# Kernel optimization log

Measured on AMD Instinct MI355X. Metric: run time of the kernel, lower is better.

Reference implementation:

```python
import jax, jax.numpy as jnp
import numpy as np

N = 50000          # nodes
E = 1_600_000      # directed edges (avg degree 32)
C_IN = 512
C_OUT = 64
H1, F1 = 8, 8      # conv1: heads=8, out per head=8
H2 = 1             # conv2: heads_2=1, concat=False
NEG_SLOPE = 0.2    # GATConv default leaky_relu slope
ELU_ALPHA = 0.2    # F.elu(..., alpha=0.2) in forward


def _glorot(key, shape):
    fan_in, fan_out = shape[0], shape[-1]
    lim = jnp.sqrt(6.0 / (fan_in + fan_out))
    return jax.random.uniform(key, shape, jnp.float32, -lim, lim)


def setup_inputs() -> dict:
    key = jax.random.key(0)
    ks = jax.random.split(key, 12)
    x = jax.random.normal(ks[0], (N, C_IN), jnp.float32)
    edge_index = jax.random.randint(ks[1], (2, E), 0, N, jnp.int32)
    # conv1 params
    W1 = _glorot(ks[2], (C_IN, H1 * F1))
    att_src1 = _glorot(ks[3], (H1, F1))
    att_dst1 = _glorot(ks[4], (H1, F1))
    b1 = jnp.zeros((H1 * F1,), jnp.float32)
    # conv2 params (concat=False, heads=1)
    W2 = _glorot(ks[5], (H1 * F1, H2 * C_OUT))
    att_src2 = _glorot(ks[6], (H2, C_OUT))
    att_dst2 = _glorot(ks[7], (H2, C_OUT))
    b2 = jnp.zeros((C_OUT,), jnp.float32)
    return dict(x=x, edge_index=edge_index, W1=W1, att_src1=att_src1,
                att_dst1=att_dst1, b1=b1, W2=W2, att_src2=att_src2,
                att_dst2=att_dst2, b2=b2)


def gat_conv(x, src, dst, W, att_src, att_dst, bias, concat):
    """PyG GATConv (self-loops already appended to src/dst). Eval mode (no dropout)."""
    n = x.shape[0]
    H, F = att_src.shape
    h = (x @ W).reshape(n, H, F)                       # [N,H,F]
    a_src = jnp.sum(h * att_src, axis=-1)              # [N,H]
    a_dst = jnp.sum(h * att_dst, axis=-1)              # [N,H]
    e = jax.nn.leaky_relu(a_src[src] + a_dst[dst], NEG_SLOPE)  # [E',H]
    # segment softmax over incoming edges of each destination node
    m = jax.ops.segment_max(e, dst, num_segments=n)    # [N,H]
    m = jnp.where(jnp.isfinite(m), m, 0.0)
    ex = jnp.exp(e - m[dst])
    denom = jax.ops.segment_sum(ex, dst, num_segments=n)
    alpha = ex / (denom[dst] + 1e-16)                  # [E',H]
    msg = h[src] * alpha[:, :, None]                   # [E',H,F]
    out = jax.ops.segment_sum(msg, dst, num_segments=n)  # [N,H,F]
    out = out.reshape(n, H * F) if concat else out.mean(axis=1)
    return out + bias


def reference(x, edge_index, W1, att_src1, att_dst1, b1,
              W2, att_src2, att_dst2, b2):
    # add self loops once (GATConv default add_self_loops=True)
    loop = jnp.arange(N, dtype=edge_index.dtype)
    src = jnp.concatenate([edge_index[0], loop])
    dst = jnp.concatenate([edge_index[1], loop])
    # dropout layers are identity in eval mode
    h = gat_conv(x, src, dst, W1, att_src1, att_dst1, b1, concat=True)
    h = jax.nn.elu(h, alpha=ELU_ALPHA)
    out = gat_conv(h, src, dst, W2, att_src2, att_dst2, b2, concat=False)
    return out
```

## Files before the change

### kernel.cpp

```cpp
#include <hip/hip_runtime.h>
#include <hip/hip_bf16.h>
#include <hip/hip_fp16.h>

constexpr int NN   = 50000;
constexpr int NE   = 1600000;
constexpr int CIN  = 512;
constexpr int DH   = 64;
constexpr int H1N  = 8;

constexpr int NB     = 98;
constexpr int TILE   = 8192;
constexpr int NTILES = (NE + TILE - 1) / TILE;
constexpr int BCAP   = 20480;

typedef __attribute__((ext_vector_type(8))) short bf16x8v;
typedef __attribute__((ext_vector_type(4))) float f32x4v;

__device__ __forceinline__ float bf(unsigned short u) {
    union { unsigned int i; float f; } v; v.i = ((unsigned int)u) << 16; return v.f;
}
__device__ __forceinline__ float lrelu(float x) { return fmaxf(x, 0.2f * x); }
__device__ __forceinline__ float ldf(const unsigned short* p, size_t i, bool f32) {
    return f32 ? ((const float*)p)[i] : bf(p[i]);
}
__device__ __forceinline__ unsigned short f2bf(float f) {
    union { float f; unsigned int u; } v; v.f = f;
    unsigned int r = (v.u + 0x7fff + ((v.u >> 16) & 1)) >> 16;
    return (unsigned short)r;
}

__global__ __launch_bounds__(256) void gat_detect(const unsigned short* __restrict__ W1,
                                                  int* __restrict__ flag) {
    __shared__ int cnt;
    if (threadIdx.x == 0) cnt = 0;
    __syncthreads();
    int local = 0;
    for (int i = threadIdx.x; i < 4096; i += 256) {
        unsigned short u = W1[i];
        int e = (u >> 7) & 0xFF;
        if (e >= 140) local++;
    }
    atomicAdd(&cnt, local);
    __syncthreads();
    if (threadIdx.x == 0) flag[0] = (cnt > 100) ? 1 : 0;
}


__global__ __launch_bounds__(256) void gat_bucketA(const int* __restrict__ src,
                                                   const int* __restrict__ dst,
                                                   int* __restrict__ gcnt,
                                                   unsigned int* __restrict__ bucketed) {
    __shared__ int hist[NB];
    __shared__ int cur[NB];
    int t = threadIdx.x;
    if (t < NB) hist[t] = 0;
    __syncthreads();
    int base = blockIdx.x * TILE;
    for (int i = t; i < TILE; i += 256) {
        int e = base + i;
        if (e < NE) atomicAdd(&hist[dst[e] >> 9], 1);
    }
    __syncthreads();
    if (t < NB) cur[t] = hist[t] ? atomicAdd(&gcnt[t], hist[t]) : 0;
    __syncthreads();
    for (int i = t; i < TILE; i += 256) {
        int e = base + i;
        if (e < NE) {
            int d = dst[e];
            int b = d >> 9;
            int p = atomicAdd(&cur[b], 1);
            if (p < BCAP)
                bucketed[(size_t)b * BCAP + p] =
                    ((unsigned int)(d & 511) << 16) | (unsigned int)src[e];
        }
    }
}

__global__ __launch_bounds__(128) void gat_bucketscan(const int* __restrict__ gcnt,
                                                      int* __restrict__ boff,
                                                      int* __restrict__ row_ptr) {
    __shared__ int s[128];
    int t = threadIdx.x;
    s[t] = (t < NB) ? gcnt[t] : 0;
    __syncthreads();
    for (int off = 1; off < 128; off <<= 1) {
        int x = s[t];
        int add = (t >= off) ? s[t - off] : 0;
        __syncthreads();
        s[t] = x + add;
        __syncthreads();
    }
    if (t <= NB) boff[t] = (t == 0) ? 0 : s[t - 1];
    if (t == 0) row_ptr[NN] = NE;
}

__global__ __launch_bounds__(256) void gat_bucketB(const unsigned int* __restrict__ bucketed,
                                                   const int* __restrict__ gcnt,
                                                   const int* __restrict__ boff,
                                                   int* __restrict__ row_ptr,
                                                   int* __restrict__ col_idx) {
    __shared__ int hist[512];
    __shared__ int sums[256];
    int t = threadIdx.x;
    int b = blockIdx.x;
    int e0 = boff[b];
    int cnt = gcnt[b]; if (cnt > BCAP) cnt = BCAP;
    const unsigned int* bb = bucketed + (size_t)b * BCAP;
    hist[t] = 0; hist[t + 256] = 0;
    __syncthreads();
    for (int i = t; i < cnt; i += 256)
        atomicAdd(&hist[bb[i] >> 16], 1);
    __syncthreads();
    int a0 = hist[2 * t], a1 = hist[2 * t + 1];
    sums[t] = a0 + a1;
    __syncthreads();
    for (int off = 1; off < 256; off <<= 1) {
        int x = sums[t];
        int add = (t >= off) ? sums[t - off] : 0;
        __syncthreads();
        sums[t] = x + add;
        __syncthreads();
    }
    int excl = (t == 0) ? 0 : sums[t - 1];
    hist[2 * t]     = excl;
    hist[2 * t + 1] = excl + a0;
    int node0 = b << 9;
    if (node0 + 2 * t     < NN) row_ptr[node0 + 2 * t]     = e0 + excl;
    if (node0 + 2 * t + 1 < NN) row_ptr[node0 + 2 * t + 1] = e0 + excl + a0;
    __syncthreads();
    for (int i = t; i < cnt; i += 256) {
        unsigned int pk = bb[i];
        int p = atomicAdd(&hist[pk >> 16], 1);
        col_idx[e0 + p] = (int)(pk & 0xFFFFu);
    }
}


__global__ __launch_bounds__(256) void gat_maxcol(const float* __restrict__ v, int n, int H,
                                                  unsigned int* __restrict__ out) {
    __shared__ float red[256];
    int t = threadIdx.x;
    float mx = -3.4e38f;
    for (int idx = blockIdx.x * 256 + t; idx < n; idx += gridDim.x * 256)
        mx = fmaxf(mx, v[idx]);
    red[t] = mx;
    __syncthreads();
    for (int off = 128; off >= H; off >>= 1) {
        if (t < off) red[t] = fmaxf(red[t], red[t + off]);
        __syncthreads();
    }
    if (t < H) {
        union { float f; unsigned int u; } b; b.f = red[t];
        unsigned int enc = (b.u & 0x80000000u) ? ~b.u : (b.u | 0x80000000u);
        atomicMax(&out[t], enc);
    }
}

__device__ __forceinline__ float gdecode(unsigned int u) {
    union { unsigned int u; float f; } d;
    d.u = (u & 0x80000000u) ? (u ^ 0x80000000u) : ~u;
    return d.f;
}


__global__ __launch_bounds__(256) void gat_transW(const unsigned short* __restrict__ W1,
                                                  const int* __restrict__ flag,
                                                  unsigned short* __restrict__ wts) {
    int idx = blockIdx.x * 256 + threadIdx.x;
    int n = idx >> 9, k = idx & 511;
    if (flag[0] == 0) {
        int o  = n * 1024 + k * 2;
        int os = o ^ ((n & 7) << 4);
        wts[os >> 1] = W1[(size_t)k * DH + n];
    } else {
        float v = ((const float*)W1)[(size_t)k * DH + n];
        unsigned short hi = f2bf(v);
        union { unsigned int u; float f; } hf; hf.u = ((unsigned int)hi) << 16;
        unsigned short lo = f2bf(v - hf.f);
        int q = k >> 7, kk = k & 127;
        int o = q * 32768 + n * 256 + ((kk * 2) ^ ((n & 7) << 4));
        wts[o >> 1]             = hi;
        wts[(o + 16384) >> 1]   = lo;
    }
}


__global__ __launch_bounds__(256) void gat_transW2(const unsigned short* __restrict__ W2,
                                                   const int* __restrict__ flag,
                                                   unsigned short* __restrict__ wts2) {
    int idx = blockIdx.x * 256 + threadIdx.x;
    if (idx >= 4096) return;
    int n = idx & 63, k = idx >> 6;
    unsigned short hi, lo;
    if (flag[0] == 0) {
        hi = W2[(size_t)k * DH + n];
        lo = 0;
    } else {
        float v = ((const float*)W2)[(size_t)k * DH + n];
        hi = f2bf(v);
        union { unsigned int u; float f; } hf; hf.u = ((unsigned int)hi) << 16;
        lo = f2bf(v - hf.f);
    }
    int o = n * 128 + ((k * 2) ^ ((n & 7) << 4));
    wts2[o >> 1]            = hi;
    wts2[(o + 8192) >> 1]   = lo;
}


__global__ __launch_bounds__(256) void gat_gemm1_mfma(const unsigned short* __restrict__ x,
                                                      const unsigned short* __restrict__ wts,
                                                      const unsigned short* __restrict__ as1,
                                                      const unsigned short* __restrict__ ad1,
                                                      const int* __restrict__ flag,
                                                      __half* __restrict__ h1h,
                                                      float* __restrict__ a_s1,
                                                      float* __restrict__ a_d1) {
    if (flag[0] != 0) return;
    __shared__ __align__(16) unsigned short wl[32768];
    int t = threadIdx.x;
#pragma unroll
    for (int it = 0; it < 16; ++it) {
        int c = it * 256 + t;
        *(uint4*)((char*)wl + c * 16) = *(const uint4*)((const char*)wts + c * 16);
    }
    __syncthreads();

    int lane = t & 63, wv = t >> 6;
    int g = lane >> 4;
    int r = lane & 15;
    int chunk = blockIdx.x * 4 + wv;
    if (chunk * 16 >= NN) return;
    int rowbase = chunk * 16;

    int vbase = r * 1024;
    int gx = g * 16;
    int xr = (r & 7) << 4;

    const char* xrow = (const char*)x + ((size_t)(rowbase + r) * CIN + g * 8) * 2;

    f32x4v acc[4];
#pragma unroll
    for (int nt = 0; nt < 4; ++nt) acc[nt] = (f32x4v){0.f, 0.f, 0.f, 0.f};

#pragma unroll 4
    for (int s = 0; s < 16; ++s) {
        union { uint4 u; bf16x8v v; } a;
        a.u = *(const uint4*)(xrow + s * 64);
        int o = vbase + ((s * 64 + gx) ^ xr);
        const char* bp = (const char*)wl + o;
#pragma unroll
        for (int nt = 0; nt < 4; ++nt) {
            union { uint4 u; bf16x8v v; } bv;
            bv.u = *(const uint4*)(bp + nt * 16384);
            acc[nt] = __builtin_amdgcn_mfma_f32_16x16x32_bf16(a.v, bv.v, acc[nt], 0, 0, 0);
        }
    }

    float avs[4], avd[4];
#pragma unroll
    for (int nt = 0; nt < 4; ++nt) {
        avs[nt] = bf(as1[nt * 16 + r]);
        avd[nt] = bf(ad1[nt * 16 + r]);
    }

#pragma unroll
    for (int nt = 0; nt < 4; ++nt) {
#pragma unroll
        for (int i = 0; i < 4; ++i) {
            int row = rowbase + g * 4 + i;
            float v = acc[nt][i];
            h1h[(size_t)row * DH + nt * 16 + r] = __float2half(v);
            float ps = v * avs[nt];
            float pd = v * avd[nt];
            ps += __shfl_xor(ps, 1, 64); ps += __shfl_xor(ps, 2, 64); ps += __shfl_xor(ps, 4, 64);
            pd += __shfl_xor(pd, 1, 64); pd += __shfl_xor(pd, 2, 64); pd += __shfl_xor(pd, 4, 64);
            if ((r & 7) == 0) {
                int head = nt * 2 + (r >> 3);
                a_s1[row * H1N + head] = ps;
                a_d1[row * H1N + head] = pd;
            }
        }
    }
}


__global__ __launch_bounds__(256) void gat_gemm1_mfma_f32(const float* __restrict__ x,
                                                          const unsigned short* __restrict__ wts,
                                                          const float* __restrict__ as1,
                                                          const float* __restrict__ ad1,
                                                          const int* __restrict__ flag,
                                                          __half* __restrict__ h1h,
                                                          float* __restrict__ a_s1,
                                                          float* __restrict__ a_d1) {
    if (flag[0] == 0) return;
    __shared__ __align__(16) unsigned short wl[16384];
    int t = threadIdx.x;
    int lane = t & 63, wv = t >> 6;
    int g = lane >> 4;
    int r = lane & 15;
    int chunk = blockIdx.x * 4 + wv;
    bool active = (chunk * 16 < NN);
    int rowbase = (active ? chunk : 0) * 16;

    int vbase = r * 256;
    int xr = (r & 7) << 4;

    const float* xrow = x + (size_t)(rowbase + r) * CIN + g * 8;

    f32x4v acc[4];
#pragma unroll
    for (int nt = 0; nt < 4; ++nt) acc[nt] = (f32x4v){0.f, 0.f, 0.f, 0.f};

    for (int q = 0; q < 4; ++q) {
        if (q) __syncthreads();
        const uint4* gsrc = (const uint4*)((const char*)wts + q * 32768);
#pragma unroll
        for (int it = 0; it < 8; ++it)
            ((uint4*)wl)[it * 256 + t] = gsrc[it * 256 + t];
        __syncthreads();

#pragma unroll
        for (int s = 0; s < 4; ++s) {
            const float4* xp = (const float4*)(xrow + q * 128 + s * 32);
            float4 v0 = xp[0], v1 = xp[1];
            float xv[8] = {v0.x, v0.y, v0.z, v0.w, v1.x, v1.y, v1.z, v1.w};
            union { unsigned short u[8]; bf16x8v v; } ahi, alo;
#pragma unroll
            for (int i2 = 0; i2 < 8; ++i2) {
                union { float f; unsigned int u; } xb; xb.f = xv[i2];
                unsigned int hb = xb.u & 0xffff0000u;
                union { unsigned int u; float f; } hf; hf.u = hb;
                ahi.u[i2] = (unsigned short)(xb.u >> 16);
                alo.u[i2] = f2bf(xv[i2] - hf.f);
            }
            int o = vbase + ((s * 64 + g * 16) ^ xr);
#pragma unroll
            for (int nt = 0; nt < 4; ++nt) {
                union { uint4 u; bf16x8v v; } bhi, blo;
                bhi.u = *(const uint4*)((const char*)wl + nt * 4096 + o);
                blo.u = *(const uint4*)((const char*)wl + 16384 + nt * 4096 + o);
                acc[nt] = __builtin_amdgcn_mfma_f32_16x16x32_bf16(ahi.v, bhi.v, acc[nt], 0, 0, 0);
                acc[nt] = __builtin_amdgcn_mfma_f32_16x16x32_bf16(ahi.v, blo.v, acc[nt], 0, 0, 0);
                acc[nt] = __builtin_amdgcn_mfma_f32_16x16x32_bf16(alo.v, bhi.v, acc[nt], 0, 0, 0);
            }
        }
    }

    if (!active) return;

    float avs[4], avd[4];
#pragma unroll
    for (int nt = 0; nt < 4; ++nt) {
        avs[nt] = as1[nt * 16 + r];
        avd[nt] = ad1[nt * 16 + r];
    }

#pragma unroll
    for (int nt = 0; nt < 4; ++nt) {
#pragma unroll
        for (int i = 0; i < 4; ++i) {
            int row = rowbase + g * 4 + i;
            float v = acc[nt][i];
            h1h[(size_t)row * DH + nt * 16 + r] = __float2half(v);
            float ps = v * avs[nt];
            float pd = v * avd[nt];
            ps += __shfl_xor(ps, 1, 64); ps += __shfl_xor(ps, 2, 64); ps += __shfl_xor(ps, 4, 64);
            pd += __shfl_xor(pd, 1, 64); pd += __shfl_xor(pd, 2, 64); pd += __shfl_xor(pd, 4, 64);
            if ((r & 7) == 0) {
                int head = nt * 2 + (r >> 3);
                a_s1[row * H1N + head] = ps;
                a_d1[row * H1N + head] = pd;
            }
        }
    }
}


__global__ __launch_bounds__(256) void gat_agg1(const int* __restrict__ row_ptr,
                                                const int* __restrict__ col_idx,
                                                const float* __restrict__ a_s1,
                                                const float* __restrict__ a_d1,
                                                const unsigned int* __restrict__ Gsu,
                                                const __half* __restrict__ h1h,
                                                const unsigned short* __restrict__ b1,
                                                const int* __restrict__ flag,
                                                float* __restrict__ hout) {
    const bool f32 = (flag[0] != 0);
    int i = (blockIdx.x * 256 + threadIdx.x) >> 6;
    int lane = threadIdx.x & 63;
    if (i >= NN) return;
    int ek = lane & 3;
    int eh = (lane >> 2) & 7;
    int wbase = (lane >> 3) << 2;

    float adst = a_d1[i * H1N + eh];
    float m = lrelu(gdecode(Gsu[eh]) + adst);

    int jb = row_ptr[i], je = row_ptr[i + 1];
    int deg = je - jb;
    int myidx = (lane < deg) ? col_idx[jb + lane] : 0;

    float wself = __expf(lrelu(a_s1[i * H1N + eh] + adst) - m);
    float denp = (ek == 0) ? wself : 0.f;
    float wsb = __shfl(wself, wbase, 64);
    float acc = wsb * __half2float(h1h[(size_t)i * DH + lane]);

    for (int j0 = 0; j0 < deg; j0 += 4) {
        int s0, s1, s2, s3, se;
        bool vE = (j0 + ek) < deg;
        if (j0 < 64) {
            s0 = __shfl(myidx, j0,     64);
            s1 = __shfl(myidx, j0 + 1, 64);
            s2 = __shfl(myidx, j0 + 2, 64);
            s3 = __shfl(myidx, j0 + 3, 64);
            se = __shfl(myidx, j0 + ek, 64);
        } else {
            int j1 = j0 + 1 < deg ? j0 + 1 : j0;
            int j2 = j0 + 2 < deg ? j0 + 2 : j0;
            int j3 = j0 + 3 < deg ? j0 + 3 : j0;
            int jve = vE ? (j0 + ek) : j0;
            s0 = col_idx[jb + j0];
            s1 = col_idx[jb + j1];
            s2 = col_idx[jb + j2];
            s3 = col_idx[jb + j3];
            se = col_idx[jb + jve];
        }
        float w = __expf(lrelu(a_s1[se * H1N + eh] + adst) - m);
        w = vE ? w : 0.f;
        denp += w;
        float w0 = __shfl(w, wbase + 0, 64);
        float w1 = __shfl(w, wbase + 1, 64);
        float w2 = __shfl(w, wbase + 2, 64);
        float w3 = __shfl(w, wbase + 3, 64);
        float r0 = __half2float(h1h[(size_t)s0 * DH + lane]);
        float r1 = __half2float(h1h[(size_t)s1 * DH + lane]);
        float r2 = __half2float(h1h[(size_t)s2 * DH + lane]);
        float r3 = __half2float(h1h[(size_t)s3 * DH + lane]);
        acc += (w0 * r0 + w1 * r1) + (w2 * r2 + w3 * r3);
    }
    denp += __shfl_xor(denp, 1, 64);
    denp += __shfl_xor(denp, 2, 64);
    float denom = __shfl(denp, wbase, 64);

    float val = acc / denom + ldf(b1, lane, f32);
    val = val > 0.f ? val : 0.2f * (__expf(val) - 1.f);
    hout[(size_t)i * DH + lane] = val;
}


__global__ __launch_bounds__(256) void gat_gemm2_mfma(const float* __restrict__ hin,
                                                      const unsigned short* __restrict__ wts2,
                                                      const unsigned short* __restrict__ as2,
                                                      const unsigned short* __restrict__ ad2,
                                                      const int* __restrict__ flag,
                                                      __half* __restrict__ h2h,
                                                      float* __restrict__ a_s2,
                                                      float* __restrict__ a_d2) {
    __shared__ __align__(16) unsigned short wl[8192];
    const bool f32 = (flag[0] != 0);
    int t = threadIdx.x;
#pragma unroll
    for (int it = 0; it < 4; ++it)
        ((uint4*)wl)[it * 256 + t] = ((const uint4*)wts2)[it * 256 + t];
    __syncthreads();

    int lane = t & 63, wv = t >> 6;
    int g = lane >> 4;
    int r = lane & 15;
    int chunk = blockIdx.x * 4 + wv;
    if (chunk * 16 >= NN) return;
    int rowbase = chunk * 16;

    int vbase = r * 128;
    int xr = (r & 7) << 4;

    const float* xrow = hin + (size_t)(rowbase + r) * DH + g * 8;

    f32x4v acc[4];
#pragma unroll
    for (int nt = 0; nt < 4; ++nt) acc[nt] = (f32x4v){0.f, 0.f, 0.f, 0.f};

#pragma unroll
    for (int s = 0; s < 2; ++s) {
        const float4* xp = (const float4*)(xrow + s * 32);
        float4 v0 = xp[0], v1 = xp[1];
        float xv[8] = {v0.x, v0.y, v0.z, v0.w, v1.x, v1.y, v1.z, v1.w};
        union { unsigned short u[8]; bf16x8v v; } ahi, alo;
#pragma unroll
        for (int i2 = 0; i2 < 8; ++i2) {
            union { float f; unsigned int u; } xb; xb.f = xv[i2];
            unsigned int hb = xb.u & 0xffff0000u;
            union { unsigned int u; float f; } hf; hf.u = hb;
            ahi.u[i2] = (unsigned short)(xb.u >> 16);
            alo.u[i2] = f2bf(xv[i2] - hf.f);
        }
        int o = vbase + ((s * 64 + g * 16) ^ xr);
#pragma unroll
        for (int nt = 0; nt < 4; ++nt) {
            union { uint4 u; bf16x8v v; } bhi, blo;
            bhi.u = *(const uint4*)((const char*)wl + nt * 2048 + o);
            blo.u = *(const uint4*)((const char*)wl + 8192 + nt * 2048 + o);
            acc[nt] = __builtin_amdgcn_mfma_f32_16x16x32_bf16(ahi.v, bhi.v, acc[nt], 0, 0, 0);
            acc[nt] = __builtin_amdgcn_mfma_f32_16x16x32_bf16(ahi.v, blo.v, acc[nt], 0, 0, 0);
            acc[nt] = __builtin_amdgcn_mfma_f32_16x16x32_bf16(alo.v, bhi.v, acc[nt], 0, 0, 0);
        }
    }

    float avs[4], avd[4];
#pragma unroll
    for (int nt = 0; nt < 4; ++nt) {
        avs[nt] = ldf(as2, nt * 16 + r, f32);
        avd[nt] = ldf(ad2, nt * 16 + r, f32);
    }

#pragma unroll
    for (int i = 0; i < 4; ++i) {
        int row = rowbase + g * 4 + i;
        float ps = 0.f, pd = 0.f;
#pragma unroll
        for (int nt = 0; nt < 4; ++nt) {
            float v = acc[nt][i];
            h2h[(size_t)row * DH + nt * 16 + r] = __float2half(v);
            ps += v * avs[nt];
            pd += v * avd[nt];
        }
        ps += __shfl_xor(ps, 1, 64); ps += __shfl_xor(ps, 2, 64);
        ps += __shfl_xor(ps, 4, 64); ps += __shfl_xor(ps, 8, 64);
        pd += __shfl_xor(pd, 1, 64); pd += __shfl_xor(pd, 2, 64);
        pd += __shfl_xor(pd, 4, 64); pd += __shfl_xor(pd, 8, 64);
        if (r == 0) { a_s2[row] = ps; a_d2[row] = pd; }
    }
}


__global__ __launch_bounds__(256) void gat_agg2(const int* __restrict__ row_ptr,
                                                const int* __restrict__ col_idx,
                                                const float* __restrict__ a_s2,
                                                const float* __restrict__ a_d2,
                                                const unsigned int* __restrict__ Gsu2,
                                                const __half* __restrict__ h2h,
                                                const unsigned short* __restrict__ b2,
                                                const int* __restrict__ flag,
                                                void* __restrict__ out) {
    const bool f32 = (flag[0] != 0);
    int i = (blockIdx.x * 256 + threadIdx.x) >> 6;
    int lane = threadIdx.x & 63;
    if (i >= NN) return;
    int ek = lane & 3;

    float adst = a_d2[i];
    float m = lrelu(gdecode(Gsu2[0]) + adst);

    int jb = row_ptr[i], je = row_ptr[i + 1];
    int deg = je - jb;
    int myidx = (lane < deg) ? col_idx[jb + lane] : 0;

    float wself = __expf(lrelu(a_s2[i] + adst) - m);
    float denp = (ek == 0) ? wself : 0.f;
    float acc = wself * __half2float(h2h[(size_t)i * DH + lane]);

    for (int j0 = 0; j0 < deg; j0 += 4) {
        int s0, s1, s2, s3, se;
        bool vE = (j0 + ek) < deg;
        if (j0 < 64) {
            s0 = __shfl(myidx, j0,     64);
            s1 = __shfl(myidx, j0 + 1, 64);
            s2 = __shfl(myidx, j0 + 2, 64);
            s3 = __shfl(myidx, j0 + 3, 64);
            se = __shfl(myidx, j0 + ek, 64);
        } else {
            int j1 = j0 + 1 < deg ? j0 + 1 : j0;
            int j2 = j0 + 2 < deg ? j0 + 2 : j0;
            int j3 = j0 + 3 < deg ? j0 + 3 : j0;
            int jve = vE ? (j0 + ek) : j0;
            s0 = col_idx[jb + j0];
            s1 = col_idx[jb + j1];
            s2 = col_idx[jb + j2];
            s3 = col_idx[jb + j3];
            se = col_idx[jb + jve];
        }
        float w = __expf(lrelu(a_s2[se] + adst) - m);
        w = vE ? w : 0.f;
        denp += w;
        float w0 = __shfl(w, 0, 64);
        float w1 = __shfl(w, 1, 64);
        float w2 = __shfl(w, 2, 64);
        float w3 = __shfl(w, 3, 64);
        float r0 = __half2float(h2h[(size_t)s0 * DH + lane]);
        float r1 = __half2float(h2h[(size_t)s1 * DH + lane]);
        float r2 = __half2float(h2h[(size_t)s2 * DH + lane]);
        float r3 = __half2float(h2h[(size_t)s3 * DH + lane]);
        acc += (w0 * r0 + w1 * r1) + (w2 * r2 + w3 * r3);
    }
    denp += __shfl_xor(denp, 1, 64);
    denp += __shfl_xor(denp, 2, 64);
    float denom = __shfl(denp, 0, 64);

    float val = acc / denom + ldf(b2, lane, f32);
    size_t oi = (size_t)i * DH + lane;
    if (f32) ((float*)out)[oi] = val;
    else     ((__hip_bfloat16*)out)[oi] = __float2bfloat16(val);
}


static void* g_scratch = nullptr;

extern "C" void kernel_launch(void* const* d_in, const int* in_sizes, int n_in,
                              void* d_out, int out_size, void* d_ws, size_t ws_size,
                              hipStream_t stream) {
    const unsigned short* x   = (const unsigned short*)d_in[0];
    const int*            ei  = (const int*)d_in[1];
    const unsigned short* W1  = (const unsigned short*)d_in[2];
    const unsigned short* as1 = (const unsigned short*)d_in[3];
    const unsigned short* ad1 = (const unsigned short*)d_in[4];
    const unsigned short* b1  = (const unsigned short*)d_in[5];
    const unsigned short* W2  = (const unsigned short*)d_in[6];
    const unsigned short* as2 = (const unsigned short*)d_in[7];
    const unsigned short* ad2 = (const unsigned short*)d_in[8];
    const unsigned short* b2  = (const unsigned short*)d_in[9];

    const int* srcv = ei;
    const int* dstv = ei + NE;

    const size_t off_wts   = 64;
    const size_t off_wts2  = off_wts + 131072;
    const size_t off_h1h   = off_wts2 + 16384;
    const size_t off_hmid  = off_h1h + (size_t)NN * DH * 2;
    const size_t off_as1   = off_hmid + (size_t)NN * DH * 4;
    const size_t off_ad1   = off_as1 + (size_t)NN * H1N * 4;
    const size_t off_rp    = off_ad1 + (size_t)NN * H1N * 4;
    const size_t off_ci    = off_rp + (size_t)(NN + 1) * 4;
    const size_t off_bk    = off_ci + (size_t)NE * 4;
    const size_t off_gcnt  = off_bk + (size_t)NB * BCAP * 4;
    const size_t off_gsu   = off_gcnt + 128 * 4;
    const size_t off_boff  = off_gsu + 16 * 4;
    const size_t need      = off_boff + 128 * 4;

    void* wsbase = d_ws;
    if (ws_size < need) {
        if (g_scratch == nullptr) hipMalloc(&g_scratch, need);
        wsbase = g_scratch;
    }
    char* B = (char*)wsbase;

    int*            flag = (int*)B;
    unsigned short* wts  = (unsigned short*)(B + off_wts);
    unsigned short* wts2 = (unsigned short*)(B + off_wts2);
    __half*         h1h  = (__half*)(B + off_h1h);
    float*          hmid = (float*)(B + off_hmid);
    float*          a_s1 = (float*)(B + off_as1);
    float*          a_d1 = (float*)(B + off_ad1);
    int*         row_ptr = (int*)(B + off_rp);
    int*         col_idx = (int*)(B + off_ci);
    unsigned int* bucketed = (unsigned int*)(B + off_bk);
    int*            gcnt = (int*)(B + off_gcnt);
    unsigned int*   Gsu  = (unsigned int*)(B + off_gsu);
    int*            boff = (int*)(B + off_boff);
    __half* h2h  = h1h;
    float* a_s2 = a_s1;
    float* a_d2 = a_d1;

    hipMemsetAsync(gcnt, 0, (128 + 16) * sizeof(int), stream);
    gat_detect<<<1, 256, 0, stream>>>(W1, flag);

    gat_bucketA   <<<NTILES, 256, 0, stream>>>(srcv, dstv, gcnt, bucketed);
    gat_bucketscan<<<1, 128, 0, stream>>>(gcnt, boff, row_ptr);
    gat_bucketB   <<<NB, 256, 0, stream>>>(bucketed, gcnt, boff, row_ptr, col_idx);

    gat_transW <<<128, 256, 0, stream>>>(W1, flag, wts);
    gat_transW2<<<16, 256, 0, stream>>>(W2, flag, wts2);
    int gemmb = (3125 + 3) / 4;
    gat_gemm1_mfma    <<<gemmb, 256, 0, stream>>>(x, wts, as1, ad1, flag, h1h, a_s1, a_d1);
    gat_gemm1_mfma_f32<<<gemmb, 256, 0, stream>>>((const float*)x, wts,
                                                  (const float*)as1, (const float*)ad1,
                                                  flag, h1h, a_s1, a_d1);

    gat_maxcol<<<64, 256, 0, stream>>>(a_s1, NN * H1N, 8, Gsu);

    int nb = (NN * 64 + 255) / 256;
    gat_agg1<<<nb, 256, 0, stream>>>(row_ptr, col_idx, a_s1, a_d1, Gsu, h1h, b1, flag, hmid);

    gat_gemm2_mfma<<<gemmb, 256, 0, stream>>>(hmid, wts2, as2, ad2, flag, h2h, a_s2, a_d2);

    gat_maxcol<<<32, 256, 0, stream>>>(a_s2, NN, 1, Gsu + 8);

    gat_agg2<<<nb, 256, 0, stream>>>(row_ptr, col_idx, a_s2, a_d2, Gsu + 8, h2h, b2, flag, d_out);
}
```

Baseline: 420.6 us.

## Split aggregation into four source-range passes for gather locality

The CSR build now sub-sorts each destination's edges by source quarter and records four row-pointer segments per node. Each aggregation kernel runs four times, each pass handling only neighbours from one quarter of the source range. Partial denominators and accumulators are carried between passes in global memory. The aim is a smaller gathered working set of h and attention scores per pass, so it fits better in cache, at the cost of extra launches, extra partial-state reads and writes, and loss of the shuffle-based index broadcast.

```diff
diff --git a/kernel.cpp b/kernel.cpp
--- a/kernel.cpp
+++ b/kernel.cpp
@@ -27,6 +27,9 @@
     union { float f; unsigned int u; } v; v.f = f;
     unsigned int r = (v.u + 0x7fff + ((v.u >> 16) & 1)) >> 16;
     return (unsigned short)r;
+}
+__device__ __forceinline__ int srctile(int s) {
+    return (s >= 12500) + (s >= 25000) + (s >= 37500);
 }
 
 __global__ __launch_bounds__(256) void gat_detect(const unsigned short* __restrict__ W1,
@@ -78,7 +81,7 @@
 
 __global__ __launch_bounds__(128) void gat_bucketscan(const int* __restrict__ gcnt,
                                                       int* __restrict__ boff,
-                                                      int* __restrict__ row_ptr) {
+                                                      int* __restrict__ rp2) {
     __shared__ int s[128];
     int t = threadIdx.x;
     s[t] = (t < NB) ? gcnt[t] : 0;
@@ -91,28 +94,34 @@
         __syncthreads();
     }
     if (t <= NB) boff[t] = (t == 0) ? 0 : s[t - 1];
-    if (t == 0) row_ptr[NN] = NE;
-}
+    if (t == 0) rp2[NN * 4] = NE;
+}
+
 
 __global__ __launch_bounds__(256) void gat_bucketB(const unsigned int* __restrict__ bucketed,
                                                    const int* __restrict__ gcnt,
                                                    const int* __restrict__ boff,
-                                                   int* __restrict__ row_ptr,
+                                                   int* __restrict__ rp2,
                                                    int* __restrict__ col_idx) {
-    __shared__ int hist[512];
+    __shared__ int hist[2048];
     __shared__ int sums[256];
     int t = threadIdx.x;
     int b = blockIdx.x;
     int e0 = boff[b];
     int cnt = gcnt[b]; if (cnt > BCAP) cnt = BCAP;
     const unsigned int* bb = bucketed + (size_t)b * BCAP;
-    hist[t] = 0; hist[t + 256] = 0;
-    __syncthreads();
-    for (int i = t; i < cnt; i += 256)
-        atomicAdd(&hist[bb[i] >> 16], 1);
-    __syncthreads();
-    int a0 = hist[2 * t], a1 = hist[2 * t + 1];
-    sums[t] = a0 + a1;
+    for (int z = t; z < 2048; z += 256) hist[z] = 0;
+    __syncthreads();
+    for (int i = t; i < cnt; i += 256) {
+        unsigned int pk = bb[i];
+        int sv = (int)(pk & 0xFFFFu);
+        atomicAdd(&hist[((pk >> 16) << 2) | srctile(sv)], 1);
+    }
+    __syncthreads();
+    int loc[8]; int s = 0;
+#pragma unroll
+    for (int u = 0; u < 8; ++u) { loc[u] = hist[t * 8 + u]; s += loc[u]; }
+    sums[t] = s;
     __syncthreads();
     for (int off = 1; off < 256; off <<= 1) {
         int x = sums[t];
@@ -121,17 +130,21 @@
         sums[t] = x + add;
         __syncthreads();
     }
-    int excl = (t == 0) ? 0 : sums[t - 1];
-    hist[2 * t]     = excl;
-    hist[2 * t + 1] = excl + a0;
+    int run = (t == 0) ? 0 : sums[t - 1];
     int node0 = b << 9;
-    if (node0 + 2 * t     < NN) row_ptr[node0 + 2 * t]     = e0 + excl;
-    if (node0 + 2 * t + 1 < NN) row_ptr[node0 + 2 * t + 1] = e0 + excl + a0;
+#pragma unroll
+    for (int u = 0; u < 8; ++u) {
+        hist[t * 8 + u] = run;
+        int node = node0 + 2 * t + (u >> 2);
+        if (node < NN) rp2[node * 4 + (u & 3)] = e0 + run;
+        run += loc[u];
+    }
     __syncthreads();
     for (int i = t; i < cnt; i += 256) {
         unsigned int pk = bb[i];
-        int p = atomicAdd(&hist[pk >> 16], 1);
-        col_idx[e0 + p] = (int)(pk & 0xFFFFu);
+        int sv = (int)(pk & 0xFFFFu);
+        int p = atomicAdd(&hist[((pk >> 16) << 2) | srctile(sv)], 1);
+        col_idx[e0 + p] = sv;
     }
 }
 
@@ -376,7 +389,7 @@
 }
 
 
-__global__ __launch_bounds__(256) void gat_agg1(const int* __restrict__ row_ptr,
+__global__ __launch_bounds__(256) void gat_agg1(const int* __restrict__ rp2,
                                                 const int* __restrict__ col_idx,
                                                 const float* __restrict__ a_s1,
                                                 const float* __restrict__ a_d1,
@@ -384,7 +397,9 @@
                                                 const __half* __restrict__ h1h,
                                                 const unsigned short* __restrict__ b1,
                                                 const int* __restrict__ flag,
-                                                float* __restrict__ hout) {
+                                                float* __restrict__ denbuf,
+                                                float* __restrict__ accst,
+                                                int pass) {
     const bool f32 = (flag[0] != 0);
     int i = (blockIdx.x * 256 + threadIdx.x) >> 6;
     int lane = threadIdx.x & 63;
@@ -396,35 +411,28 @@
     float adst = a_d1[i * H1N + eh];
     float m = lrelu(gdecode(Gsu[eh]) + adst);
 
-    int jb = row_ptr[i], je = row_ptr[i + 1];
+    int jb = rp2[i * 4 + pass], je = rp2[i * 4 + pass + 1];
     int deg = je - jb;
-    int myidx = (lane < deg) ? col_idx[jb + lane] : 0;
-
-    float wself = __expf(lrelu(a_s1[i * H1N + eh] + adst) - m);
-    float denp = (ek == 0) ? wself : 0.f;
-    float wsb = __shfl(wself, wbase, 64);
-    float acc = wsb * __half2float(h1h[(size_t)i * DH + lane]);
+
+    float denp, acc;
+    if (pass == 0) {
+        float wself = __expf(lrelu(a_s1[i * H1N + eh] + adst) - m);
+        denp = (ek == 0) ? wself : 0.f;
+        float wsb = __shfl(wself, wbase, 64);
+        acc = wsb * __half2float(h1h[(size_t)i * DH + lane]);
+    } else {
+        denp = (ek == 0) ? denbuf[i * H1N + eh] : 0.f;
+        acc = accst[(size_t)i * DH + lane];
+    }
 
     for (int j0 = 0; j0 < deg; j0 += 4) {
-        int s0, s1, s2, s3, se;
+        int dm1 = deg - 1;
+        int s0 = col_idx[jb + j0];
+        int s1 = col_idx[jb + (j0 + 1 < deg ? j0 + 1 : dm1)];
+        int s2 = col_idx[jb + (j0 + 2 < deg ? j0 + 2 : dm1)];
+        int s3 = col_idx[jb + (j0 + 3 < deg ? j0 + 3 : dm1)];
+        int se = (ek == 0) ? s0 : (ek == 1) ? s1 : (ek == 2) ? s2 : s3;
         bool vE = (j0 + ek) < deg;
-        if (j0 < 64) {
-            s0 = __shfl(myidx, j0,     64);
-            s1 = __shfl(myidx, j0 + 1, 64);
-            s2 = __shfl(myidx, j0 + 2, 64);
-            s3 = __shfl(myidx, j0 + 3, 64);
-            se = __shfl(myidx, j0 + ek, 64);
-        } else {
-            int j1 = j0 + 1 < deg ? j0 + 1 : j0;
-            int j2 = j0 + 2 < deg ? j0 + 2 : j0;
-            int j3 = j0 + 3 < deg ? j0 + 3 : j0;
-            int jve = vE ? (j0 + ek) : j0;
-            s0 = col_idx[jb + j0];
-            s1 = col_idx[jb + j1];
-            s2 = col_idx[jb + j2];
-            s3 = col_idx[jb + j3];
-            se = col_idx[jb + jve];
-        }
         float w = __expf(lrelu(a_s1[se * H1N + eh] + adst) - m);
         w = vE ? w : 0.f;
         denp += w;
@@ -440,11 +448,16 @@
     }
     denp += __shfl_xor(denp, 1, 64);
     denp += __shfl_xor(denp, 2, 64);
-    float denom = __shfl(denp, wbase, 64);
-
-    float val = acc / denom + ldf(b1, lane, f32);
-    val = val > 0.f ? val : 0.2f * (__expf(val) - 1.f);
-    hout[(size_t)i * DH + lane] = val;
+
+    if (pass < 3) {
+        if (ek == 0) denbuf[i * H1N + eh] = denp;
+        accst[(size_t)i * DH + lane] = acc;
+    } else {
+        float denom = __shfl(denp, wbase, 64);
+        float val = acc / denom + ldf(b1, lane, f32);
+        val = val > 0.f ? val : 0.2f * (__expf(val) - 1.f);
+        accst[(size_t)i * DH + lane] = val;
+    }
 }
 
 
@@ -533,7 +546,7 @@
 }
 
 
-__global__ __launch_bounds__(256) void gat_agg2(const int* __restrict__ row_ptr,
+__global__ __launch_bounds__(256) void gat_agg2(const int* __restrict__ rp2,
                                                 const int* __restrict__ col_idx,
                                                 const float* __restrict__ a_s2,
                                                 const float* __restrict__ a_d2,
@@ -541,7 +554,10 @@
                                                 const __half* __restrict__ h2h,
                                                 const unsigned short* __restrict__ b2,
                                                 const int* __restrict__ flag,
-                                                void* __restrict__ out) {
+                                                float* __restrict__ denbuf,
+                                                float* __restrict__ accst,
+                                                void* __restrict__ out,
+                                                int pass) {
     const bool f32 = (flag[0] != 0);
     int i = (blockIdx.x * 256 + threadIdx.x) >> 6;
     int lane = threadIdx.x & 63;
@@ -551,34 +567,27 @@
     float adst = a_d2[i];
     float m = lrelu(gdecode(Gsu2[0]) + adst);
 
-    int jb = row_ptr[i], je = row_ptr[i + 1];
+    int jb = rp2[i * 4 + pass], je = rp2[i * 4 + pass + 1];
     int deg = je - jb;
-    int myidx = (lane < deg) ? col_idx[jb + lane] : 0;
-
-    float wself = __expf(lrelu(a_s2[i] + adst) - m);
-    float denp = (ek == 0) ? wself : 0.f;
-    float acc = wself * __half2float(h2h[(size_t)i * DH + lane]);
+
+    float denp, acc;
+    if (pass == 0) {
+        float wself = __expf(lrelu(a_s2[i] + adst) - m);
+        denp = (ek == 0) ? wself : 0.f;
+        acc = __shfl(wself, 0, 64) * __half2float(h2h[(size_t)i * DH + lane]);
+    } else {
+        denp = (ek == 0) ? denbuf[i] : 0.f;
+        acc = accst[(size_t)i * DH + lane];
+    }
 
     for (int j0 = 0; j0 < deg; j0 += 4) {
-        int s0, s1, s2, s3, se;
+        int dm1 = deg - 1;
+        int s0 = col_idx[jb + j0];
+        int s1 = col_idx[jb + (j0 + 1 < deg ? j0 + 1 : dm1)];
+        int s2 = col_idx[jb + (j0 + 2 < deg ? j0 + 2 : dm1)];
+        int s3 = col_idx[jb + (j0 + 3 < deg ? j0 + 3 : dm1)];
+        int se = (ek == 0) ? s0 : (ek == 1) ? s1 : (ek == 2) ? s2 : s3;
         bool vE = (j0 + ek) < deg;
-        if (j0 < 64) {
-            s0 = __shfl(myidx, j0,     64);
-            s1 = __shfl(myidx, j0 + 1, 64);
-            s2 = __shfl(myidx, j0 + 2, 64);
-            s3 = __shfl(myidx, j0 + 3, 64);
-            se = __shfl(myidx, j0 + ek, 64);
-        } else {
-            int j1 = j0 + 1 < deg ? j0 + 1 : j0;
-            int j2 = j0 + 2 < deg ? j0 + 2 : j0;
-            int j3 = j0 + 3 < deg ? j0 + 3 : j0;
-            int jve = vE ? (j0 + ek) : j0;
-            s0 = col_idx[jb + j0];
-            s1 = col_idx[jb + j1];
-            s2 = col_idx[jb + j2];
-            s3 = col_idx[jb + j3];
-            se = col_idx[jb + jve];
-        }
         float w = __expf(lrelu(a_s2[se] + adst) - m);
         w = vE ? w : 0.f;
         denp += w;
@@ -594,12 +603,17 @@
     }
     denp += __shfl_xor(denp, 1, 64);
     denp += __shfl_xor(denp, 2, 64);
-    float denom = __shfl(denp, 0, 64);
-
-    float val = acc / denom + ldf(b2, lane, f32);
-    size_t oi = (size_t)i * DH + lane;
-    if (f32) ((float*)out)[oi] = val;
-    else     ((__hip_bfloat16*)out)[oi] = __float2bfloat16(val);
+
+    if (pass < 3) {
+        if (ek == 0 && lane < 4) denbuf[i] = denp;
+        accst[(size_t)i * DH + lane] = acc;
+    } else {
+        float denom = __shfl(denp, 0, 64);
+        float val = acc / denom + ldf(b2, lane, f32);
+        size_t oi = (size_t)i * DH + lane;
+        if (f32) ((float*)out)[oi] = val;
+        else     ((__hip_bfloat16*)out)[oi] = __float2bfloat16(val);
+    }
 }
 
 
@@ -628,8 +642,9 @@
     const size_t off_hmid  = off_h1h + (size_t)NN * DH * 2;
     const size_t off_as1   = off_hmid + (size_t)NN * DH * 4;
     const size_t off_ad1   = off_as1 + (size_t)NN * H1N * 4;
-    const size_t off_rp    = off_ad1 + (size_t)NN * H1N * 4;
-    const size_t off_ci    = off_rp + (size_t)(NN + 1) * 4;
+    const size_t off_den   = off_ad1 + (size_t)NN * H1N * 4;
+    const size_t off_rp2   = off_den + (size_t)NN * H1N * 4;
+    const size_t off_ci    = off_rp2 + ((size_t)NN * 4 + 1) * 4;
     const size_t off_bk    = off_ci + (size_t)NE * 4;
     const size_t off_gcnt  = off_bk + (size_t)NB * BCAP * 4;
     const size_t off_gsu   = off_gcnt + 128 * 4;
@@ -650,7 +665,8 @@
     float*          hmid = (float*)(B + off_hmid);
     float*          a_s1 = (float*)(B + off_as1);
     float*          a_d1 = (float*)(B + off_ad1);
-    int*         row_ptr = (int*)(B + off_rp);
+    float*          denb = (float*)(B + off_den);
+    int*            rp2  = (int*)(B + off_rp2);
     int*         col_idx = (int*)(B + off_ci);
     unsigned int* bucketed = (unsigned int*)(B + off_bk);
     int*            gcnt = (int*)(B + off_gcnt);
@@ -664,8 +680,8 @@
     gat_detect<<<1, 256, 0, stream>>>(W1, flag);
 
     gat_bucketA   <<<NTILES, 256, 0, stream>>>(srcv, dstv, gcnt, bucketed);
-    gat_bucketscan<<<1, 128, 0, stream>>>(gcnt, boff, row_ptr);
-    gat_bucketB   <<<NB, 256, 0, stream>>>(bucketed, gcnt, boff, row_ptr, col_idx);
+    gat_bucketscan<<<1, 128, 0, stream>>>(gcnt, boff, rp2);
+    gat_bucketB   <<<NB, 256, 0, stream>>>(bucketed, gcnt, boff, rp2, col_idx);
 
     gat_transW <<<128, 256, 0, stream>>>(W1, flag, wts);
     gat_transW2<<<16, 256, 0, stream>>>(W2, flag, wts2);
@@ -678,11 +694,15 @@
     gat_maxcol<<<64, 256, 0, stream>>>(a_s1, NN * H1N, 8, Gsu);
 
     int nb = (NN * 64 + 255) / 256;
-    gat_agg1<<<nb, 256, 0, stream>>>(row_ptr, col_idx, a_s1, a_d1, Gsu, h1h, b1, flag, hmid);
+    for (int p = 0; p < 4; ++p)
+        gat_agg1<<<nb, 256, 0, stream>>>(rp2, col_idx, a_s1, a_d1, Gsu, h1h, b1, flag,
+                                         denb, hmid, p);
 
     gat_gemm2_mfma<<<gemmb, 256, 0, stream>>>(hmid, wts2, as2, ad2, flag, h2h, a_s2, a_d2);
 
     gat_maxcol<<<32, 256, 0, stream>>>(a_s2, NN, 1, Gsu + 8);
 
-    gat_agg2<<<nb, 256, 0, stream>>>(row_ptr, col_idx, a_s2, a_d2, Gsu + 8, h2h, b2, flag, d_out);
-}
+    for (int p = 0; p < 4; ++p)
+        gat_agg2<<<nb, 256, 0, stream>>>(rp2, col_idx, a_s2, a_d2, Gsu + 8, h2h, b2, flag,
+                                         denb, hmid, d_out, p);
+}
```

Result: slower. 527.7 us (+25.5%).
